# Kernel optimization log

Hardware: AMD Instinct MI355X
Metric: run time of the kernel (lower is better)

The kernel has to match this reference:

```python
import jax, jax.numpy as jnp
import numpy as np

B, N, DIM = 2, 512, 128
HEADS, DH = 4, 64
INNER = HEADS * DH            # 256
POS_HID = 64
MULT = 4                      # attn_mlp_hidden_mult
K = 16                        # num_neighbors


def setup_inputs() -> dict:
    key = jax.random.key(0)
    ks = jax.random.split(key, 10)
    w = lambda k, shape: jax.random.normal(k, shape, jnp.float32) * 0.02
    return {
        "x": jax.random.normal(ks[0], (B, N, DIM), jnp.float32),
        "pos": jax.random.normal(ks[1], (B, N, 3), jnp.float32),
        "mask": jnp.ones((B, N), dtype=bool),
        "w_qkv": w(ks[2], (DIM, 3 * INNER)),
        "w_out": w(ks[3], (INNER, DIM)),
        "b_out": jnp.zeros((DIM,), jnp.float32),
        "w_pos1": w(ks[4], (3, POS_HID)),
        "b_pos1": jnp.zeros((POS_HID,), jnp.float32),
        "w_pos2": w(ks[5], (POS_HID, INNER)),
        "b_pos2": jnp.zeros((INNER,), jnp.float32),
        # grouped 1x1 convs == per-head linear layers
        "w_attn1": w(ks[6], (HEADS, DH, MULT * DH)),
        "b_attn1": jnp.zeros((HEADS, MULT * DH), jnp.float32),
        "w_attn2": w(ks[7], (HEADS, MULT * DH, DH)),
        "b_attn2": jnp.zeros((HEADS, DH), jnp.float32),
    }


def reference(x, pos, mask, w_qkv, w_out, b_out, w_pos1, b_pos1, w_pos2, b_pos2,
              w_attn1, b_attn1, w_attn2, b_attn2):
    b, n, _ = x.shape
    h, d = HEADS, DH

    qkv = x @ w_qkv                                   # [b, n, 3*inner]
    q, k, v = jnp.split(qkv, 3, axis=-1)
    to_heads = lambda t: t.reshape(b, n, h, d).transpose(0, 2, 1, 3)  # b h n d
    q, k, v = map(to_heads, (q, k, v))

    # dense pairwise relative positions + pos MLP  [b, n, n, inner]
    rel_pos = pos[:, :, None, :] - pos[:, None, :, :]            # [b, n, n, 3]
    rpe = jax.nn.relu(rel_pos @ w_pos1 + b_pos1) @ w_pos2 + b_pos2

    # masked topk over pairwise distance (smallest K)
    rel_dist = jnp.linalg.norm(rel_pos, axis=-1)                 # [b, n, n]
    mask2 = mask[:, :, None] & mask[:, None, :]                  # [b, n, n]
    fmax = jnp.finfo(rel_dist.dtype).max
    rel_dist = jnp.where(mask2, rel_dist, fmax)
    _, idx = jax.lax.top_k(-rel_dist, K)                         # [b, n, K]

    # neighbor gathers (equivalent to torch batched_index_select over j)
    gather_hd = jax.vmap(lambda t, i: t[:, i, :])                # [h,n,d],[n,K] -> [h,n,K,d]
    k_nb = gather_hd(k, idx)                                     # [b, h, n, K, d]
    v_nb = gather_hd(v, idx)
    row = jnp.arange(n)[:, None]
    rpe_nb = jax.vmap(lambda r, i: r[row, i])(rpe, idx)          # [b, n, K, inner]
    rpe_nb = rpe_nb.reshape(b, n, K, h, d).transpose(0, 3, 1, 2, 4)  # [b,h,n,K,d]
    mask_nb = jax.vmap(lambda m, i: m[row, i])(mask2, idx)       # [b, n, K]

    # qk_rel gathered implicitly: (q_i - k_j)[j=idx] == q_i - k_nb
    attn_in = q[:, :, :, None, :] - k_nb + rpe_nb                # [b, h, n, K, d]

    # grouped 1x1 conv MLP == per-head MLP on last dim
    hid = jax.nn.relu(jnp.einsum('bhikd,hde->bhike', attn_in, w_attn1)
                      + b_attn1[None, :, None, None, :])
    sim = (jnp.einsum('bhike,hed->bhikd', hid, w_attn2)
           + b_attn2[None, :, None, None, :])                    # [b, h, n, K, d]

    sim = jnp.where(mask_nb[:, None, :, :, None], sim, -fmax)
    # torch: sim is [b, (h d), i, j]; softmax(dim=-2) is over i -> axis 2 here
    attn = jax.nn.softmax(sim, axis=2)

    v_full = v_nb + rpe_nb                                       # [b, h, n, K, d]
    agg = jnp.sum(attn * v_full, axis=3)                         # [b, h, n, d]
    agg = agg.transpose(0, 2, 1, 3).reshape(b, n, h * d)         # [b, n, inner]
    return agg @ w_out + b_out
```

## Files before the change

kernel.cpp:

```cpp
#include <hip/hip_runtime.h>

#define B_ 2
#define N_ 512
#define DIM_ 128
#define HEADS_ 4
#define DH_ 64
#define INNER_ 256
#define PH_ 64
#define HID2_ 256
#define KNB_ 16

typedef unsigned long long u64;
typedef unsigned int u32;
typedef unsigned short u16;
typedef __attribute__((ext_vector_type(8))) short bf16x8;
typedef __attribute__((ext_vector_type(8))) unsigned short us8;
typedef __attribute__((ext_vector_type(4))) float f32x4;

__device__ __forceinline__ float bf2f(u16 u) {
    union { float f; u32 u; } c; c.u = ((u32)u) << 16; return c.f;
}
__device__ __forceinline__ u16 f2bf(float f) {
    union { float f; u32 u; } c; c.f = f;
    u32 u = c.u;
    return (u16)((u + 0x7fffu + ((u >> 16) & 1u)) >> 16);
}
__device__ __forceinline__ u32 pack2(float lo, float hi) {
    return ((u32)f2bf(hi) << 16) | (u32)f2bf(lo);
}

__global__ __launch_bounds__(256) void k_front(
        const float* __restrict__ x, const float* __restrict__ pos, const float* __restrict__ w_qkv,
        const float* __restrict__ w_a1, const float* __restrict__ w_a2, const float* __restrict__ w_p2,
        u16* __restrict__ wf1, u16* __restrict__ wf2, u16* __restrict__ wfp,
        u16* __restrict__ qb, u16* __restrict__ kb, float* __restrict__ v,
        int* __restrict__ idx) {
    int blk = blockIdx.x;
    if (blk < 576) {
        int t = blk * 256 + threadIdx.x;
        if (t < 65536) {
            int jj = t & 7, lbig = (t >> 3) & 63, f = t >> 9;
            int s = f & 1, etL = (f >> 1) & 7, half = (f >> 4) & 1, h = f >> 5;
            int lr = lbig & 15, g = lbig >> 4;
            int d = s * 32 + g * 8 + jj, e = (half * 8 + etL) * 16 + lr;
            wf1[t] = f2bf(w_a1[((h * 64 + d) << 8) + e]);
        } else if (t < 131072) {
            int t2 = t - 65536;
            int jj = t2 & 7, lbig = (t2 >> 3) & 63, f = t2 >> 9;
            int s = f & 7, ct = (f >> 3) & 3, h = f >> 5;
            int lr = lbig & 15, g = lbig >> 4;
            int e = s * 32 + g * 8 + jj, c = ct * 16 + lr;
            wf2[t2] = f2bf(w_a2[(((h << 8) + e) << 6) + c]);
        } else {
            int t3 = t - 131072;
            int jj = t3 & 7, lbig = (t3 >> 3) & 63, f = t3 >> 9;
            int s = f & 1, ct = (f >> 1) & 3, h = f >> 3;
            int lr = lbig & 15, g = lbig >> 4;
            int e = s * 32 + g * 8 + jj, c = h * 64 + ct * 16 + lr;
            wfp[t3] = f2bf(w_p2[(e << 8) + c]);
        }
    } else if (blk < 704) {
        int bu = blk - 576;
        int b = bu >> 6;
        int n0 = (bu & 63) * 8;
        int t = threadIdx.x;
        __shared__ float xs[8][128];
        #pragma unroll
        for (int p = 0; p < 4; ++p) {
            int e = p * 256 + t;
            xs[e >> 7][e & 127] = x[((size_t)(b * N_ + n0) + (e >> 7)) * DIM_ + (e & 127)];
        }
        __syncthreads();
        float acc[3][8];
        #pragma unroll
        for (int cc = 0; cc < 3; ++cc)
            #pragma unroll
            for (int r = 0; r < 8; ++r) acc[cc][r] = 0.f;
        for (int c4 = 0; c4 < 32; ++c4) {
            float wv[3][4];
            #pragma unroll
            for (int dd = 0; dd < 4; ++dd)
                #pragma unroll
                for (int cc = 0; cc < 3; ++cc)
                    wv[cc][dd] = w_qkv[(size_t)(c4 * 4 + dd) * (3 * INNER_) + cc * INNER_ + t];
            #pragma unroll
            for (int r = 0; r < 8; ++r) {
                float4 xv = *(const float4*)&xs[r][c4 * 4];
                #pragma unroll
                for (int cc = 0; cc < 3; ++cc)
                    acc[cc][r] += xv.x * wv[cc][0] + xv.y * wv[cc][1] + xv.z * wv[cc][2] + xv.w * wv[cc][3];
            }
        }
        int h = t >> 6, d = t & 63;
        #pragma unroll
        for (int r = 0; r < 8; ++r) {
            size_t o = (((size_t)(b * HEADS_ + h)) * N_ + n0 + r) * DH_ + d;
            qb[o] = f2bf(acc[0][r]);
            kb[o] = f2bf(acc[1][r]);
            v[o]  = acc[2][r];
        }
    } else {
        int wave = (blk - 704) * 4 + (threadIdx.x >> 6);
        int lane = threadIdx.x & 63;
        int b = wave >> 9;
        float px = pos[(size_t)wave * 3 + 0];
        float py = pos[(size_t)wave * 3 + 1];
        float pz = pos[(size_t)wave * 3 + 2];
        u64 keys[8];
        #pragma unroll
        for (int s = 0; s < 8; ++s) {
            int j = s * 64 + lane;
            float dx = __fsub_rn(px, pos[(size_t)(b * N_ + j) * 3 + 0]);
            float dy = __fsub_rn(py, pos[(size_t)(b * N_ + j) * 3 + 1]);
            float dz = __fsub_rn(pz, pos[(size_t)(b * N_ + j) * 3 + 2]);
            float s2 = __fadd_rn(__fadd_rn(__fmul_rn(dx, dx), __fmul_rn(dy, dy)), __fmul_rn(dz, dz));
            float dist = __fsqrt_rn(s2);
            keys[s] = ((u64)__float_as_uint(dist) << 32) | (unsigned)j;
        }
        for (int r = 0; r < KNB_; ++r) {
            u64 m = keys[0];
            #pragma unroll
            for (int s = 1; s < 8; ++s) m = (keys[s] < m) ? keys[s] : m;
            #pragma unroll
            for (int off = 32; off >= 1; off >>= 1) {
                u64 o = __shfl_xor(m, off);
                m = (o < m) ? o : m;
            }
            if (lane == 0) idx[(size_t)wave * KNB_ + r] = (int)(m & 0xffffffffu);
            #pragma unroll
            for (int s = 0; s < 8; ++s) if (keys[s] == m) keys[s] = ~0ull;
        }
    }
}

__global__ __launch_bounds__(256, 2) void k_attn(
        const u16* __restrict__ qb, const u16* __restrict__ kb, const float* __restrict__ v,
        const int* __restrict__ idx,
        const float* __restrict__ pos, const float* __restrict__ w_p1, const float* __restrict__ b_p1,
        const float* __restrict__ b_p2, const u16* __restrict__ wfp,
        const u16* __restrict__ wf1, const u16* __restrict__ wf2,
        const float* __restrict__ b_a1, const float* __restrict__ b_a2,
        u16* __restrict__ sim, u16* __restrict__ vf) {
    __shared__ u16 HID[4][2][16 * 136];
    int t = threadIdx.x;
    int wv = t >> 6, l = t & 63, lr = l & 15, g = l >> 4;
    int blk = blockIdx.x;
    int bh = blk >> 6;
    int b = bh >> 2, h = bh & 3;
    int i0 = (blk & 63) * 8 + wv * 2;

    float rx[2], ry[2], rz[2];
    us8 qv[2][2], kv[2][2];
    float4 v0[2][2], v1[2][2];
    #pragma unroll
    for (int ii = 0; ii < 2; ++ii) {
        int i = i0 + ii, bi = (b << 9) + i;
        int j = idx[(bi << 4) + lr];
        int bj = (b << 9) + j;
        rx[ii] = pos[(size_t)bi * 3 + 0] - pos[(size_t)bj * 3 + 0];
        ry[ii] = pos[(size_t)bi * 3 + 1] - pos[(size_t)bj * 3 + 1];
        rz[ii] = pos[(size_t)bi * 3 + 2] - pos[(size_t)bj * 3 + 2];
        #pragma unroll
        for (int s = 0; s < 2; ++s) {
            qv[ii][s] = *(const us8*)&qb[(size_t)(bh * N_ + i) * 64 + s * 32 + g * 8];
            kv[ii][s] = *(const us8*)&kb[(size_t)(bh * N_ + j) * 64 + s * 32 + g * 8];
            v0[ii][s] = *(const float4*)&v[(size_t)(bh * N_ + j) * 64 + s * 32 + g * 8];
            v1[ii][s] = *(const float4*)&v[(size_t)(bh * N_ + j) * 64 + s * 32 + g * 8 + 4];
        }
    }

    bf16x8 hidp[2][2];
    #pragma unroll
    for (int ii = 0; ii < 2; ++ii) {
        #pragma unroll
        for (int s = 0; s < 2; ++s) {
            u16 tmp[8];
            #pragma unroll
            for (int jj = 0; jj < 8; ++jj) {
                int e = s * 32 + g * 8 + jj;
                float hh = b_p1[e] + rx[ii] * w_p1[e] + ry[ii] * w_p1[PH_ + e] + rz[ii] * w_p1[2 * PH_ + e];
                tmp[jj] = f2bf(fmaxf(hh, 0.f));
            }
            hidp[ii][s] = *(bf16x8*)tmp;
        }
    }

    {
        bf16x8 Ar[4][2];
        #pragma unroll
        for (int ct = 0; ct < 4; ++ct)
            #pragma unroll
            for (int s = 0; s < 2; ++s)
                Ar[ct][s] = *(const bf16x8*)&wfp[(size_t)((((h << 2) + ct) << 1) + s) * 512 + l * 8];
        #pragma unroll
        for (int ct = 0; ct < 4; ++ct) {
            f32x4 C0 = {0.f, 0.f, 0.f, 0.f}, C1 = {0.f, 0.f, 0.f, 0.f};
            #pragma unroll
            for (int s = 0; s < 2; ++s) {
                C0 = __builtin_amdgcn_mfma_f32_16x16x32_bf16(Ar[ct][s], hidp[0][s], C0, 0, 0, 0);
                C1 = __builtin_amdgcn_mfma_f32_16x16x32_bf16(Ar[ct][s], hidp[1][s], C1, 0, 0, 0);
            }
            float4 bias = *(const float4*)&b_p2[h * 64 + ct * 16 + g * 4];
            uint2 o0, o1;
            o0.x = pack2(C0[0] + bias.x, C0[1] + bias.y);
            o0.y = pack2(C0[2] + bias.z, C0[3] + bias.w);
            o1.x = pack2(C1[0] + bias.x, C1[1] + bias.y);
            o1.y = pack2(C1[2] + bias.z, C1[3] + bias.w);
            *(uint2*)&HID[wv][0][lr * 136 + ct * 16 + g * 4] = o0;
            *(uint2*)&HID[wv][1][lr * 136 + ct * 16 + g * 4] = o1;
        }
    }

    bf16x8 ain[2][2];
    #pragma unroll
    for (int ii = 0; ii < 2; ++ii) {
        int i = i0 + ii;
        #pragma unroll
        for (int s = 0; s < 2; ++s) {
            bf16x8 rp = *(const bf16x8*)&HID[wv][ii][lr * 136 + s * 32 + g * 8];
            us8 rpu = *(const us8*)&rp;
            float vvr[8] = {v0[ii][s].x, v0[ii][s].y, v0[ii][s].z, v0[ii][s].w,
                            v1[ii][s].x, v1[ii][s].y, v1[ii][s].z, v1[ii][s].w};
            u16 ta[8], tv[8];
            #pragma unroll
            for (int jj = 0; jj < 8; ++jj) {
                float rpf = bf2f(rpu[jj]);
                ta[jj] = f2bf(bf2f(qv[ii][s][jj]) - bf2f(kv[ii][s][jj]) + rpf);
                tv[jj] = f2bf(vvr[jj] + rpf);
            }
            ain[ii][s] = *(bf16x8*)ta;
            *(bf16x8*)&vf[(size_t)(((bh * N_ + i) << 4) + lr) * 64 + s * 32 + g * 8] = *(bf16x8*)tv;
        }
    }

    f32x4 C2[2][4];
    #pragma unroll
    for (int ii = 0; ii < 2; ++ii)
        #pragma unroll
        for (int ct = 0; ct < 4; ++ct) C2[ii][ct] = (f32x4){0.f, 0.f, 0.f, 0.f};
    #pragma unroll
    for (int half = 0; half < 2; ++half) {
        bf16x8 A1[8][2];
        #pragma unroll
        for (int etL = 0; etL < 8; ++etL)
            #pragma unroll
            for (int s = 0; s < 2; ++s)
                A1[etL][s] = *(const bf16x8*)&wf1[(size_t)(((((h << 1) + half) << 3) + etL) * 2 + s) * 512 + l * 8];
        #pragma unroll
        for (int etL = 0; etL < 8; ++etL) {
            int et = half * 8 + etL;
            f32x4 C0 = {0.f, 0.f, 0.f, 0.f}, C1 = {0.f, 0.f, 0.f, 0.f};
            #pragma unroll
            for (int s = 0; s < 2; ++s) {
                C0 = __builtin_amdgcn_mfma_f32_16x16x32_bf16(A1[etL][s], ain[0][s], C0, 0, 0, 0);
                C1 = __builtin_amdgcn_mfma_f32_16x16x32_bf16(A1[etL][s], ain[1][s], C1, 0, 0, 0);
            }
            float4 bias = *(const float4*)&b_a1[h * 256 + et * 16 + g * 4];
            uint2 p0, p1;
            p0.x = pack2(fmaxf(C0[0] + bias.x, 0.f), fmaxf(C0[1] + bias.y, 0.f));
            p0.y = pack2(fmaxf(C0[2] + bias.z, 0.f), fmaxf(C0[3] + bias.w, 0.f));
            p1.x = pack2(fmaxf(C1[0] + bias.x, 0.f), fmaxf(C1[1] + bias.y, 0.f));
            p1.y = pack2(fmaxf(C1[2] + bias.z, 0.f), fmaxf(C1[3] + bias.w, 0.f));
            *(uint2*)&HID[wv][0][lr * 136 + etL * 16 + g * 4] = p0;
            *(uint2*)&HID[wv][1][lr * 136 + etL * 16 + g * 4] = p1;
        }
        #pragma unroll
        for (int chunk = 0; chunk < 2; ++chunk) {
            bf16x8 A2[4][2];
            #pragma unroll
            for (int ct = 0; ct < 4; ++ct)
                #pragma unroll
                for (int ss = 0; ss < 2; ++ss) {
                    int s = half * 4 + chunk * 2 + ss;
                    A2[ct][ss] = *(const bf16x8*)&wf2[(size_t)((((h << 2) + ct) << 3) + s) * 512 + l * 8];
                }
            #pragma unroll
            for (int ss = 0; ss < 2; ++ss) {
                int sL = chunk * 2 + ss;
                bf16x8 B0 = *(const bf16x8*)&HID[wv][0][lr * 136 + sL * 32 + g * 8];
                bf16x8 B1 = *(const bf16x8*)&HID[wv][1][lr * 136 + sL * 32 + g * 8];
                #pragma unroll
                for (int ct = 0; ct < 4; ++ct) {
                    C2[0][ct] = __builtin_amdgcn_mfma_f32_16x16x32_bf16(A2[ct][ss], B0, C2[0][ct], 0, 0, 0);
                    C2[1][ct] = __builtin_amdgcn_mfma_f32_16x16x32_bf16(A2[ct][ss], B1, C2[1][ct], 0, 0, 0);
                }
            }
        }
    }
    #pragma unroll
    for (int ii = 0; ii < 2; ++ii) {
        int i = i0 + ii;
        #pragma unroll
        for (int ct = 0; ct < 4; ++ct) {
            float4 bias = *(const float4*)&b_a2[h * 64 + ct * 16 + g * 4];
            uint2 o;
            o.x = pack2(C2[ii][ct][0] + bias.x, C2[ii][ct][1] + bias.y);
            o.y = pack2(C2[ii][ct][2] + bias.z, C2[ii][ct][3] + bias.w);
            *(uint2*)&sim[(size_t)(((bh * N_ + i) << 4) + lr) * 64 + ct * 16 + g * 4] = o;
        }
    }
}

__global__ __launch_bounds__(256) void k_stats(const u16* __restrict__ sim, float* __restrict__ R) {
    int blk = blockIdx.x;
    int ks = blk & 15, bh = blk >> 4;
    int d0 = (threadIdx.x & 15) * 4;
    int nc = threadIdx.x >> 4;
    __shared__ float red[16][69];
    size_t base = ((size_t)(bh * N_ + nc * 32) * 16 + ks) * 64 + d0;
    float s0 = 0.f, s1 = 0.f, s2 = 0.f, s3 = 0.f;
    for (int nn = 0; nn < 32; ++nn) {
        uint2 u = *(const uint2*)&sim[base + (size_t)nn * 1024];
        s0 += __expf(bf2f((u16)(u.x & 0xffff)));
        s1 += __expf(bf2f((u16)(u.x >> 16)));
        s2 += __expf(bf2f((u16)(u.y & 0xffff)));
        s3 += __expf(bf2f((u16)(u.y >> 16)));
    }
    red[nc][d0 + 0] = s0; red[nc][d0 + 1] = s1;
    red[nc][d0 + 2] = s2; red[nc][d0 + 3] = s3;
    __syncthreads();
    int t = threadIdx.x;
    if (t < 64) {
        float s = 0.f;
        #pragma unroll
        for (int c = 0; c < 16; ++c) s += red[c][t];
        R[(size_t)blk * 64 + t] = 1.f / s;
    }
}

__global__ __launch_bounds__(256) void k_agg_out(
        const u16* __restrict__ sim, const u16* __restrict__ vf, const float* __restrict__ R,
        const float* __restrict__ w, const float* __restrict__ bo, float* __restrict__ out) {
    int blk = blockIdx.x;
    int b = blk >> 7;
    int i0 = (blk & 127) * 4;
    int t = threadIdx.x;
    __shared__ float ag[4][260];
    {
        int h = t >> 6, d = t & 63;
        int bh = b * HEADS_ + h;
        float Rk[16];
        #pragma unroll
        for (int ks = 0; ks < 16; ++ks) Rk[ks] = R[((bh << 4) + ks) * 64 + d];
        #pragma unroll
        for (int r = 0; r < 4; ++r) {
            size_t base = (size_t)((bh * N_ + i0 + r) << 4) * 64 + d;
            float acc = 0.f;
            #pragma unroll
            for (int ks = 0; ks < 16; ++ks) {
                float p = __expf(bf2f(sim[base + (size_t)ks * 64])) * Rk[ks];
                acc += p * bf2f(vf[base + (size_t)ks * 64]);
            }
            ag[r][h * 64 + d] = acc;
        }
    }
    __syncthreads();
    int c = t & 127, rg = t >> 7;
    float acc[2];
    acc[0] = bo[c]; acc[1] = bo[c];
    for (int k4 = 0; k4 < 64; ++k4) {
        float wv[4];
        #pragma unroll
        for (int kk = 0; kk < 4; ++kk) wv[kk] = w[(size_t)(k4 * 4 + kk) * DIM_ + c];
        #pragma unroll
        for (int rr = 0; rr < 2; ++rr) {
            float4 a4 = *(const float4*)&ag[rr * 2 + rg][k4 * 4];
            acc[rr] += a4.x * wv[0] + a4.y * wv[1] + a4.z * wv[2] + a4.w * wv[3];
        }
    }
    #pragma unroll
    for (int rr = 0; rr < 2; ++rr)
        out[(size_t)((b << 9) + i0 + rr * 2 + rg) * DIM_ + c] = acc[rr];
}

extern "C" void kernel_launch(void* const* d_in, const int* in_sizes, int n_in,
                              void* d_out, int out_size, void* d_ws, size_t ws_size,
                              hipStream_t stream) {
    const float* x      = (const float*)d_in[0];
    const float* pos    = (const float*)d_in[1];
    const float* w_qkv  = (const float*)d_in[3];
    const float* w_out  = (const float*)d_in[4];
    const float* b_out  = (const float*)d_in[5];
    const float* w_pos1 = (const float*)d_in[6];
    const float* b_pos1 = (const float*)d_in[7];
    const float* w_pos2 = (const float*)d_in[8];
    const float* b_pos2 = (const float*)d_in[9];
    const float* w_a1   = (const float*)d_in[10];
    const float* b_a1   = (const float*)d_in[11];
    const float* w_a2   = (const float*)d_in[12];
    const float* b_a2   = (const float*)d_in[13];
    float* out = (float*)d_out;

    char* W = (char*)d_ws;
    u16*  qb   = (u16*)W;            W += 524288;
    u16*  kb   = (u16*)W;            W += 524288;
    float* v   = (float*)W;          W += 1048576;
    int*  idx  = (int*)W;            W += 65536;
    u16*  sim  = (u16*)W;            W += 8388608;
    u16*  vf   = (u16*)W;            W += 8388608;
    float* R   = (float*)W;          W += 32768;
    u16*  wf1  = (u16*)W;            W += 131072;
    u16*  wf2  = (u16*)W;            W += 131072;
    u16*  wfp  = (u16*)W;            W += 32768;

    k_front<<<960, 256, 0, stream>>>(x, pos, w_qkv, w_a1, w_a2, w_pos2,
                                     wf1, wf2, wfp, qb, kb, v, idx);
    k_attn<<<512, 256, 0, stream>>>(qb, kb, v, idx, pos, w_pos1, b_pos1, b_pos2, wfp,
                                    wf1, wf2, b_a1, b_a2, sim, vf);
    k_stats<<<128, 256, 0, stream>>>(sim, R);
    k_agg_out<<<256, 256, 0, stream>>>(sim, vf, R, w_out, b_out, out);
}
```

Before: 61.78 us.

## Split attention kernel into separate gather and per-head MLP kernels

The fused attention kernel is split in two. A gather kernel builds the attention input and the value-plus-position tensors, assigning one head per wave so each block covers one point pair across all heads. A separate MLP kernel reads the attention input back and runs the two grouped MLP matmuls. The intent is to cut register and LDS pressure in each kernel and raise occupancy. The cost is an extra 8 MB bf16 round trip through global memory and one more kernel launch.

```diff
diff --git a/kernel.cpp b/kernel.cpp
--- a/kernel.cpp
+++ b/kernel.cpp
@@ -133,21 +133,19 @@
     }
 }
 
-__global__ __launch_bounds__(256, 2) void k_attn(
+__global__ __launch_bounds__(256) void k_gather(
         const u16* __restrict__ qb, const u16* __restrict__ kb, const float* __restrict__ v,
-        const int* __restrict__ idx,
-        const float* __restrict__ pos, const float* __restrict__ w_p1, const float* __restrict__ b_p1,
+        const int* __restrict__ idx, const float* __restrict__ pos,
+        const float* __restrict__ w_p1, const float* __restrict__ b_p1,
         const float* __restrict__ b_p2, const u16* __restrict__ wfp,
-        const u16* __restrict__ wf1, const u16* __restrict__ wf2,
-        const float* __restrict__ b_a1, const float* __restrict__ b_a2,
-        u16* __restrict__ sim, u16* __restrict__ vf) {
-    __shared__ u16 HID[4][2][16 * 136];
+        u16* __restrict__ ainb, u16* __restrict__ vf) {
+    __shared__ u16 RP[4][2][16 * 72];
     int t = threadIdx.x;
     int wv = t >> 6, l = t & 63, lr = l & 15, g = l >> 4;
     int blk = blockIdx.x;
-    int bh = blk >> 6;
-    int b = bh >> 2, h = bh & 3;
-    int i0 = (blk & 63) * 8 + wv * 2;
+    int b = blk >> 8;
+    int i0 = (blk & 255) * 2;
+    int h = wv, bh = b * HEADS_ + h;
 
     float rx[2], ry[2], rz[2];
     us8 qv[2][2], kv[2][2];
@@ -206,18 +204,17 @@
             o0.y = pack2(C0[2] + bias.z, C0[3] + bias.w);
             o1.x = pack2(C1[0] + bias.x, C1[1] + bias.y);
             o1.y = pack2(C1[2] + bias.z, C1[3] + bias.w);
-            *(uint2*)&HID[wv][0][lr * 136 + ct * 16 + g * 4] = o0;
-            *(uint2*)&HID[wv][1][lr * 136 + ct * 16 + g * 4] = o1;
-        }
-    }
-
-    bf16x8 ain[2][2];
+            *(uint2*)&RP[wv][0][lr * 72 + ct * 16 + g * 4] = o0;
+            *(uint2*)&RP[wv][1][lr * 72 + ct * 16 + g * 4] = o1;
+        }
+    }
+
     #pragma unroll
     for (int ii = 0; ii < 2; ++ii) {
         int i = i0 + ii;
         #pragma unroll
         for (int s = 0; s < 2; ++s) {
-            bf16x8 rp = *(const bf16x8*)&HID[wv][ii][lr * 136 + s * 32 + g * 8];
+            bf16x8 rp = *(const bf16x8*)&RP[wv][ii][lr * 72 + s * 32 + g * 8];
             us8 rpu = *(const us8*)&rp;
             float vvr[8] = {v0[ii][s].x, v0[ii][s].y, v0[ii][s].z, v0[ii][s].w,
                             v1[ii][s].x, v1[ii][s].y, v1[ii][s].z, v1[ii][s].w};
@@ -228,9 +225,32 @@
                 ta[jj] = f2bf(bf2f(qv[ii][s][jj]) - bf2f(kv[ii][s][jj]) + rpf);
                 tv[jj] = f2bf(vvr[jj] + rpf);
             }
-            ain[ii][s] = *(bf16x8*)ta;
+            *(bf16x8*)&ainb[(size_t)(((bh * N_ + i) << 4) + lr) * 64 + s * 32 + g * 8] = *(bf16x8*)ta;
             *(bf16x8*)&vf[(size_t)(((bh * N_ + i) << 4) + lr) * 64 + s * 32 + g * 8] = *(bf16x8*)tv;
         }
+    }
+}
+
+__global__ __launch_bounds__(256, 2) void k_mlp(
+        const u16* __restrict__ ainb,
+        const u16* __restrict__ wf1, const u16* __restrict__ wf2,
+        const float* __restrict__ b_a1, const float* __restrict__ b_a2,
+        u16* __restrict__ sim) {
+    __shared__ u16 HID[4][2][16 * 136];
+    int t = threadIdx.x;
+    int wv = t >> 6, l = t & 63, lr = l & 15, g = l >> 4;
+    int blk = blockIdx.x;
+    int bh = blk >> 6;
+    int h = bh & 3;
+    int i0 = (blk & 63) * 8 + wv * 2;
+
+    bf16x8 ain[2][2];
+    #pragma unroll
+    for (int ii = 0; ii < 2; ++ii) {
+        int i = i0 + ii;
+        #pragma unroll
+        for (int s = 0; s < 2; ++s)
+            ain[ii][s] = *(const bf16x8*)&ainb[(size_t)(((bh * N_ + i) << 4) + lr) * 64 + s * 32 + g * 8];
     }
 
     f32x4 C2[2][4];
@@ -398,6 +418,7 @@
     int*  idx  = (int*)W;            W += 65536;
     u16*  sim  = (u16*)W;            W += 8388608;
     u16*  vf   = (u16*)W;            W += 8388608;
+    u16*  ainb = (u16*)W;            W += 8388608;
     float* R   = (float*)W;          W += 32768;
     u16*  wf1  = (u16*)W;            W += 131072;
     u16*  wf2  = (u16*)W;            W += 131072;
@@ -405,8 +426,9 @@
 
     k_front<<<960, 256, 0, stream>>>(x, pos, w_qkv, w_a1, w_a2, w_pos2,
                                      wf1, wf2, wfp, qb, kb, v, idx);
-    k_attn<<<512, 256, 0, stream>>>(qb, kb, v, idx, pos, w_pos1, b_pos1, b_pos2, wfp,
-                                    wf1, wf2, b_a1, b_a2, sim, vf);
+    k_gather<<<512, 256, 0, stream>>>(qb, kb, v, idx, pos, w_pos1, b_pos1, b_pos2, wfp,
+                                      ainb, vf);
+    k_mlp<<<512, 256, 0, stream>>>(ainb, wf1, wf2, b_a1, b_a2, sim);
     k_stats<<<128, 256, 0, stream>>>(sim, R);
     k_agg_out<<<256, 256, 0, stream>>>(sim, vf, R, w_out, b_out, out);
 }
```

New measurement: 59.99 us. -2.9%, faster.
